# Performance work log

Measured on AMD Instinct MI355X. Metric: run time of the kernel, lower is better.

## Reference

```python
import jax, jax.numpy as jnp
import numpy as np

B, T, C = 2, 4096, 2048
N = 64
H = C // N
D_W, D_A, D_MV, D_G = 96, 96, 64, 256
LN_EPS = 0.00064


def setup_inputs() -> dict:
    key = jax.random.key(0)
    ks = jax.random.split(key, 32)
    rn = lambda k, shape, s=1.0: jax.random.normal(k, shape, jnp.float32) * s
    inp = {}
    inp["x"] = rn(ks[0], (B, T, C))
    inp["v_first"] = rn(ks[1], (B, T, C))
    # token-shift mixing coefficients (in (0,1) like 1 - ddd**p)
    for i, name in enumerate(["x_r", "x_w", "x_k", "x_v", "x_a", "x_g"]):
        inp[name] = jax.random.uniform(ks[2 + i], (1, 1, C), jnp.float32)
    # decay LoRA: w0 in roughly [-6, -0.5]
    inp["w0"] = jax.random.uniform(ks[8], (1, 1, C), jnp.float32, -6.0, -0.5)
    inp["w1"] = rn(ks[9], (C, D_W), 0.05)
    inp["w2"] = rn(ks[10], (D_W, C), 0.05)
    # in-context-learning-rate (a) LoRA
    inp["a0"] = rn(ks[11], (1, 1, C), 0.3) - 0.19
    inp["a1"] = rn(ks[12], (C, D_A), 0.05)
    inp["a2"] = rn(ks[13], (D_A, C), 0.05)
    # value-mix LoRA (layer_id > 0)
    inp["v0"] = rn(ks[14], (1, 1, C), 0.2) + 0.73
    inp["v1"] = rn(ks[15], (C, D_MV), 0.05)
    inp["v2"] = rn(ks[16], (D_MV, C), 0.05)
    # gate LoRA
    inp["g1"] = rn(ks[17], (C, D_G), 0.05)
    inp["g2"] = rn(ks[18], (D_G, C), 0.05)
    inp["k_k"] = rn(ks[19], (1, 1, C), 0.05) + 0.71
    inp["k_a"] = rn(ks[20], (1, 1, C), 0.02) + 1.02
    inp["r_k"] = rn(ks[21], (H, N), 0.02) - 0.04
    sc = 0.5 / C ** 0.5
    inp["W_r"] = jax.random.uniform(ks[22], (C, C), jnp.float32, -sc, sc)
    inp["W_k"] = jax.random.uniform(ks[23], (C, C), jnp.float32, -0.1 * sc, 0.1 * sc)
    inp["W_v"] = jax.random.uniform(ks[24], (C, C), jnp.float32, -sc, sc)
    inp["W_o"] = rn(ks[25], (C, C), 0.02)
    inp["ln_w"] = jnp.ones((C,), jnp.float32)
    inp["ln_b"] = jnp.zeros((C,), jnp.float32)
    return inp


def _wkv7(r, wdec, k, v, a, b):
    # r,wdec,k,v,a,b: [B,T,C]; per-head delta-rule scan, state S: [B,H,Nv,Nk]
    def heads(t):
        return t.reshape(B, T, H, N).transpose(1, 0, 2, 3)  # [T,B,H,N]

    def step(S, ins):
        r_t, w_t, k_t, v_t, a_t, b_t = ins  # each [B,H,N]
        sa = jnp.einsum('bhvk,bhk->bhv', S, a_t)
        S = (S * w_t[:, :, None, :]
             + sa[..., None] * b_t[:, :, None, :]
             + v_t[..., None] * k_t[:, :, None, :])
        y_t = jnp.einsum('bhvk,bhk->bhv', S, r_t)
        return S, y_t

    S0 = jnp.zeros((B, H, N, N), r.dtype)
    _, ys = jax.lax.scan(step, S0, (heads(r), heads(wdec), heads(k), heads(v), heads(a), heads(b)))
    return ys.transpose(1, 0, 2, 3).reshape(B, T, C)


def reference(x, v_first, x_r, x_w, x_k, x_v, x_a, x_g,
              w0, w1, w2, a0, a1, a2, v0, v1, v2, g1, g2,
              k_k, k_a, r_k, W_r, W_k, W_v, W_o, ln_w, ln_b):
    # token shift: prepend zero row, drop last
    xx = jnp.concatenate([jnp.zeros_like(x[:, :1]), x[:, :-1]], axis=1) - x
    xr = x + xx * x_r
    xw = x + xx * x_w
    xk = x + xx * x_k
    xv = x + xx * x_v
    xa = x + xx * x_a
    xg = x + xx * x_g
    r = xr @ W_r.T
    k = xk @ W_k.T
    v = xv @ W_v.T
    w = -jax.nn.softplus(-(w0 + jnp.tanh(xw @ w1) @ w2)) - 0.5
    # layer_id > 0: mix with first-layer value
    v = v + (v_first - v) * jax.nn.sigmoid(v0 + xv @ v1 @ v2)
    a = jax.nn.sigmoid(a0 + xa @ a1 @ a2)
    g = jax.nn.sigmoid(xg @ g1) @ g2
    kk = k * k_k
    kkh = kk.reshape(B, T, H, N)
    kkh = kkh / jnp.maximum(jnp.linalg.norm(kkh, axis=-1, keepdims=True), 1e-12)
    kk = kkh.reshape(B, T, C)
    k = k * (1.0 + (a - 1.0) * k_a)
    wdec = jnp.exp(-jnp.exp(w))  # RWKV7 decay parameterization
    y = _wkv7(r, wdec, k, v, -kk, kk * a)
    # GroupNorm(H groups) over channels per token
    yh = y.reshape(B, T, H, N)
    mu = yh.mean(-1, keepdims=True)
    var = yh.var(-1, keepdims=True)
    y = ((yh - mu) / jnp.sqrt(var + LN_EPS)).reshape(B, T, C) * ln_w + ln_b
    # bonus term
    rh, kh, vh = (t.reshape(B, T, H, N) for t in (r, k, v))
    bonus = ((rh * kh * r_k).sum(-1, keepdims=True) * vh).reshape(B, T, C)
    y = y + bonus
    return (y * g) @ W_o.T
```

## Files before the change

kernel.cpp:

```cpp
#include <hip/hip_runtime.h>
#include <hip/hip_bf16.h>
#include <stdint.h>
#include <math.h>

#define DEV __device__ __forceinline__

typedef __hip_bfloat16 bf16;
typedef __attribute__((ext_vector_type(8))) __bf16 bf16x8;
typedef __attribute__((ext_vector_type(4))) float f32x4;
typedef __attribute__((ext_vector_type(2))) float f32x2;

static constexpr int B_ = 2;
static constexpr int T_ = 4096;
static constexpr int C_ = 2048;
static constexpr int H_ = 32;

DEV void gld_lds16(const void* g, void* l) {
  __builtin_amdgcn_global_load_lds((const __attribute__((address_space(1))) void*)g,
                                   (__attribute__((address_space(3))) void*)l, 16, 0, 0);
}
DEV float bfbits2f(unsigned short u) {
  unsigned int x = ((unsigned int)u) << 16;
  return __builtin_bit_cast(float, x);
}
DEV unsigned short f2bfbits(float f) { bf16 h = __float2bfloat16(f); return __builtin_bit_cast(unsigned short, h); }
DEV void store_bf16x4(bf16* p, f32x4 v) {
  ushort4 u;
  u.x = f2bfbits(v.x); u.y = f2bfbits(v.y); u.z = f2bfbits(v.z); u.w = f2bfbits(v.w);
  *reinterpret_cast<ushort4*>(p) = u;
}
DEV float wsum64(float v) {
#pragma unroll
  for (int m = 32; m > 0; m >>= 1) v += __shfl_xor(v, m, 64);
  return v;
}
template<int CTRL>
DEV float dpp_add(float v) {
  int x = __builtin_bit_cast(int, v);
  int y = __builtin_amdgcn_update_dpp(0, x, CTRL, 0xf, 0xf, false);
  return v + __builtin_bit_cast(float, y);
}
DEV float red16(float v) {
  v = dpp_add<0xB1>(v);
  v = dpp_add<0x4E>(v);
  v = dpp_add<0x124>(v);
  v = dpp_add<0x128>(v);
  return v;
}
DEV f32x4 cvt4(uint2 u) {
  f32x4 o;
  o.x = __builtin_bit_cast(float, u.x << 16);
  o.y = __builtin_bit_cast(float, u.x & 0xFFFF0000u);
  o.z = __builtin_bit_cast(float, u.y << 16);
  o.w = __builtin_bit_cast(float, u.y & 0xFFFF0000u);
  return o;
}

template<int MODE>
__global__ __launch_bounds__(256)
void gemm_bt(const bf16* __restrict__ A, const bf16* __restrict__ Bm,
             void* __restrict__ Cout, const float* __restrict__ ep,
             int N, int K, int T4)
{
  __shared__ bf16 lA[128 * 64];
  __shared__ bf16 lB[128 * 64];
  const int tid  = threadIdx.x;
  const int wave = tid >> 6;
  const int lane = tid & 63;
  const long brow = (long)blockIdx.x * 128;
  const long bcol = (long)blockIdx.y * 128;
  const int wr = wave >> 1, wc = wave & 1;

  f32x4 acc[4][4];
#pragma unroll
  for (int m = 0; m < 4; ++m)
#pragma unroll
    for (int n = 0; n < 4; ++n)
      acc[m][n] = f32x4{0.f, 0.f, 0.f, 0.f};

  const bf16* pa = A  + (size_t)(brow + wave * 32 + (lane >> 3)) * K + (lane & 7) * 8;
  const bf16* pb = Bm + (size_t)(bcol + wave * 32 + (lane >> 3)) * K + (lane & 7) * 8;

  for (int k0 = 0; k0 < K; k0 += 64) {
#pragma unroll
    for (int i = 0; i < 4; ++i) gld_lds16(pa + (size_t)i * 8 * K, &lA[(wave * 4 + i) * 512]);
#pragma unroll
    for (int i = 0; i < 4; ++i) gld_lds16(pb + (size_t)i * 8 * K, &lB[(wave * 4 + i) * 512]);
    pa += 64; pb += 64;
    __syncthreads();
#pragma unroll
    for (int kk = 0; kk < 2; ++kk) {
      bf16x8 af[4], bfv[4];
#pragma unroll
      for (int m = 0; m < 4; ++m)
        af[m] = *(const bf16x8*)&lA[(wr * 64 + m * 16 + (lane & 15)) * 64 + kk * 32 + (lane >> 4) * 8];
#pragma unroll
      for (int n = 0; n < 4; ++n)
        bfv[n] = *(const bf16x8*)&lB[(wc * 64 + n * 16 + (lane & 15)) * 64 + kk * 32 + (lane >> 4) * 8];
#pragma unroll
      for (int m = 0; m < 4; ++m)
#pragma unroll
        for (int n = 0; n < 4; ++n)
          acc[m][n] = __builtin_amdgcn_mfma_f32_16x16x32_bf16(af[m], bfv[n], acc[m][n], 0, 0, 0);
    }
    __syncthreads();
  }

  const int cr = (lane >> 4) * 4;
  const int cc = lane & 15;
#pragma unroll
  for (int m = 0; m < 4; ++m) {
#pragma unroll
    for (int n = 0; n < 4; ++n) {
#pragma unroll
      for (int j = 0; j < 4; ++j) {
        long gm = brow + wr * 64 + m * 16 + cr + j;
        long gn = bcol + wc * 64 + n * 16 + cc;
        float val = acc[m][n][j];
        if constexpr (MODE == 0) {
          ((float*)Cout)[gm * N + gn] = val;
        } else if constexpr (MODE == 2) {
          ((bf16*)Cout)[gm * N + gn] = __float2bfloat16(val);
        } else if constexpr (MODE == 3) {
          ((bf16*)Cout)[gm * N + gn] = __float2bfloat16(tanhf(val));
        } else if constexpr (MODE == 4) {
          ((bf16*)Cout)[gm * N + gn] = __float2bfloat16(1.f / (1.f + expf(-val)));
        } else if constexpr (MODE == 7) {
          long b = gm / T4, t = gm % T4;
          ((bf16*)Cout)[((b * (N >> 6) + (gn >> 6)) * T4 + t) * 64 + (gn & 63)] = __float2bfloat16(val);
        } else if constexpr (MODE == 8) {
          float u = ep[gn] + val;
          float w = -log1pf(expf(-u)) - 0.5f;
          float wd = expf(-expf(w));
          long b = gm / T4, t = gm % T4;
          ((float*)Cout)[((b * (N >> 6) + (gn >> 6)) * T4 + t) * 64 + (gn & 63)] = wd;
        } else if constexpr (MODE == 9) {
          float sg = 1.f / (1.f + expf(-(ep[gn] + val)));
          long b = gm / T4, t = gm % T4;
          ((bf16*)Cout)[((b * (N >> 6) + (gn >> 6)) * T4 + t) * 64 + (gn & 63)] = __float2bfloat16(sg);
        }
      }
    }
  }
}

__global__ __launch_bounds__(256)
void mix1(const float* __restrict__ x, const float* __restrict__ coef,
          bf16* __restrict__ out)
{
  size_t e = ((size_t)blockIdx.x * 256 + threadIdx.x) * 4;
  int c = (int)(e & (C_ - 1));
  size_t m = e >> 11;
  f32x4 xc = *(const f32x4*)(x + e);
  f32x4 xp;
  if ((m & (T_ - 1)) == 0) xp = f32x4{0.f, 0.f, 0.f, 0.f};
  else                     xp = *(const f32x4*)(x + e - C_);
  f32x4 cf = *(const f32x4*)(coef + c);
  store_bf16x4(out + e, xc + (xp - xc) * cf);
}

__global__ __launch_bounds__(256)
void cvt1(const float* __restrict__ s, bf16* __restrict__ d)
{
  size_t e = ((size_t)blockIdx.x * 256 + threadIdx.x) * 4;
  store_bf16x4(d + e, *(const f32x4*)(s + e));
}

struct TPJob { const float* s; bf16* d; int R, Cs, NP, RP; };
struct TP8 { TPJob j[8]; };
__global__ __launch_bounds__(256)
void tpad(TP8 jobs)
{
  TPJob J = jobs.j[blockIdx.y];
  int i = blockIdx.x * 256 + threadIdx.x;
  int tot = J.NP * J.RP;
  if (i >= tot) return;
  int n = i / J.RP, r = i - n * J.RP;
  float v = (n < J.Cs && r < J.R) ? J.s[(size_t)r * J.Cs + n] : 0.f;
  J.d[i] = __float2bfloat16(v);
}

__global__ __launch_bounds__(256)
void prescan2(const bf16* __restrict__ r16, bf16* __restrict__ k16,
              bf16* __restrict__ v16, bf16* __restrict__ ab,
              bf16* __restrict__ vn16,
              const float* __restrict__ vfirst, const float* __restrict__ kkc,
              const float* __restrict__ kac, const float* __restrict__ rk,
              float* __restrict__ sbonus)
{
  const int wid = threadIdx.x >> 6;
  const int lane = threadIdx.x & 63;
  const long id = (long)blockIdx.x * 4 + wid;
  const long bh = id >> 12;
  const long t = id & (T_ - 1);
  const long b = bh >> 5, h = bh & (H_ - 1);
  const long mrow = b * T_ + t;
  const int c = (int)(h * 64 + lane);
  const size_t tp = (size_t)id * 64 + lane;
  float k  = __bfloat162float(k16[tp]);
  float v  = __bfloat162float(v16[tp]);
  float r  = __bfloat162float(r16[tp]);
  float a  = __bfloat162float(ab[tp]);
  float vs = __bfloat162float(vn16[tp]);
  float vf = vfirst[mrow * C_ + c];
  float kkv = k * kkc[c];
  float ssum = wsum64(kkv * kkv);
  float kkn = kkv / fmaxf(sqrtf(ssum), 1e-12f);
  float kn = k * (1.f + (a - 1.f) * kac[c]);
  float vn = v + (vf - v) * vs;
  k16[tp] = __float2bfloat16(kn);
  v16[tp] = __float2bfloat16(vn);
  ab[tp]  = __float2bfloat16(kkn * a);
  vn16[tp] = __float2bfloat16(kkn);
  float bs = wsum64(r * kn * rk[c]);
  if (lane == 0) sbonus[id] = bs;
}

struct SS {
  uint2 r0, r1, k0, k1, n0, n1, b0, b1;
  f32x4 w0, w1;
  unsigned short v0, v1;
};
DEV SS ldss(const uint2* pr, const uint2* pk, const uint2* pn, const uint2* pb,
            const f32x4* pw, const unsigned short* pv, int ss, int kq, int row)
{
  SS s;
  int i0 = ss * 32 + kq, i1 = i0 + 16;
  s.r0 = pr[i0]; s.r1 = pr[i1];
  s.k0 = pk[i0]; s.k1 = pk[i1];
  s.n0 = pn[i0]; s.n1 = pn[i1];
  s.b0 = pb[i0]; s.b1 = pb[i1];
  s.w0 = pw[i0]; s.w1 = pw[i1];
  int j0 = ss * 128 + row, j1 = j0 + 64;
  s.v0 = pv[j0]; s.v1 = pv[j1];
  return s;
}
DEV float dostep(f32x4& S, uint2 ru, uint2 ku, uint2 nu, uint2 bu,
                 f32x4 W, unsigned short vus)
{
  f32x4 R = cvt4(ru), K = cvt4(ku), N = cvt4(nu), Bv = cvt4(bu);
  float vt = bfbits2f(vus);
  f32x2 acc = S.xy * N.xy;
  acc = __builtin_elementwise_fma(S.zw, N.zw, acc);
  float sa = red16(acc.x + acc.y);
  float nsa = -sa;
  f32x2 ns2 = f32x2{nsa, nsa}, vt2 = f32x2{vt, vt};
  S.xy = __builtin_elementwise_fma(vt2, K.xy,
           __builtin_elementwise_fma(ns2, Bv.xy, S.xy * W.xy));
  S.zw = __builtin_elementwise_fma(vt2, K.zw,
           __builtin_elementwise_fma(ns2, Bv.zw, S.zw * W.zw));
  f32x2 yq = S.xy * R.xy;
  yq = __builtin_elementwise_fma(S.zw, R.zw, yq);
  return red16(yq.x + yq.y);
}
DEV void consume(f32x4& S, const SS& s, bf16* py, int t, int kq)
{
  float y0 = dostep(S, s.r0, s.k0, s.n0, s.b0, s.w0, s.v0);
  if (kq == 0) py[(size_t)t * 64] = __float2bfloat16(y0);
  float y1 = dostep(S, s.r1, s.k1, s.n1, s.b1, s.w1, s.v1);
  if (kq == 0) py[(size_t)(t + 1) * 64] = __float2bfloat16(y1);
}
__global__ __launch_bounds__(256, 1)
void wkv_scan5(const bf16* __restrict__ r16, const float* __restrict__ w32,
               const bf16* __restrict__ k16, const bf16* __restrict__ v16,
               const bf16* __restrict__ n16, const bf16* __restrict__ b16,
               bf16* __restrict__ y16)
{
  const int bh = blockIdx.x & 63;
  const int quarter = blockIdx.x >> 6;
  const int wv = threadIdx.x >> 6;
  const int lane = threadIdx.x & 63;
  const int vl = lane >> 4;
  const int kq = lane & 15;
  const int row = quarter * 16 + wv * 4 + vl;
  const size_t eb = (size_t)bh * (T_ * 64);
  const uint2* pr = (const uint2*)(r16 + eb);
  const uint2* pk = (const uint2*)(k16 + eb);
  const uint2* pn = (const uint2*)(n16 + eb);
  const uint2* pb = (const uint2*)(b16 + eb);
  const f32x4* pw = (const f32x4*)(w32 + eb);
  const unsigned short* pv = (const unsigned short*)(v16 + eb);
  bf16* py = y16 + eb + row;

  f32x4 S = f32x4{0.f, 0.f, 0.f, 0.f};
  const int NS = T_ / 2;

  SS s0 = ldss(pr, pk, pn, pb, pw, pv, 0, kq, row);
  SS s1 = ldss(pr, pk, pn, pb, pw, pv, 1, kq, row);
  SS s2 = ldss(pr, pk, pn, pb, pw, pv, 2, kq, row);
  SS s3 = ldss(pr, pk, pn, pb, pw, pv, 3, kq, row);

  for (int ss = 0; ss < NS; ss += 4) {
    int n0 = ss + 4 < NS ? ss + 4 : NS - 1;
    int n1 = ss + 5 < NS ? ss + 5 : NS - 1;
    int n2 = ss + 6 < NS ? ss + 6 : NS - 1;
    int n3 = ss + 7 < NS ? ss + 7 : NS - 1;
    SS p0 = ldss(pr, pk, pn, pb, pw, pv, n0, kq, row);
    consume(S, s0, py, 2 * ss, kq);
    SS p1 = ldss(pr, pk, pn, pb, pw, pv, n1, kq, row);
    consume(S, s1, py, 2 * ss + 2, kq);
    SS p2 = ldss(pr, pk, pn, pb, pw, pv, n2, kq, row);
    consume(S, s2, py, 2 * ss + 4, kq);
    SS p3 = ldss(pr, pk, pn, pb, pw, pv, n3, kq, row);
    consume(S, s3, py, 2 * ss + 6, kq);
    s0 = p0; s1 = p1; s2 = p2; s3 = p3;
  }
}

__global__ __launch_bounds__(256)
void postk2(const bf16* __restrict__ y16, const bf16* __restrict__ v16,
            const float* __restrict__ sbonus, const bf16* __restrict__ g16,
            const float* __restrict__ lnw, const float* __restrict__ lnb,
            bf16* __restrict__ opre)
{
  const int wid = threadIdx.x >> 6;
  const int lane = threadIdx.x & 63;
  const long id = (long)blockIdx.x * 4 + wid;
  const long bh = id >> 12;
  const long t = id & (T_ - 1);
  const long b = bh >> 5, h = bh & (H_ - 1);
  const long mrow = b * T_ + t;
  const int c = (int)(h * 64 + lane);
  const size_t tp = (size_t)id * 64 + lane;
  float y = __bfloat162float(y16[tp]);
  float mu = wsum64(y) * (1.f / 64.f);
  float d = y - mu;
  float var = wsum64(d * d) * (1.f / 64.f);
  float yn = d * rsqrtf(var + 0.00064f) * lnw[c] + lnb[c];
  float outv = (yn + sbonus[id] * __bfloat162float(v16[tp]))
               * __bfloat162float(g16[mrow * C_ + c]);
  opre[mrow * C_ + c] = __float2bfloat16(outv);
}

extern "C" void kernel_launch(void* const* d_in, const int* in_sizes, int n_in,
                              void* d_out, int out_size, void* d_ws, size_t ws_size,
                              hipStream_t stream)
{
  const float* x    = (const float*)d_in[0];
  const float* vfst = (const float*)d_in[1];
  const float* x_r  = (const float*)d_in[2];
  const float* x_w  = (const float*)d_in[3];
  const float* x_k  = (const float*)d_in[4];
  const float* x_v  = (const float*)d_in[5];
  const float* x_a  = (const float*)d_in[6];
  const float* x_g  = (const float*)d_in[7];
  const float* w0   = (const float*)d_in[8];
  const float* w1   = (const float*)d_in[9];
  const float* w2   = (const float*)d_in[10];
  const float* a0   = (const float*)d_in[11];
  const float* a1   = (const float*)d_in[12];
  const float* a2   = (const float*)d_in[13];
  const float* v0   = (const float*)d_in[14];
  const float* v1   = (const float*)d_in[15];
  const float* v2   = (const float*)d_in[16];
  const float* g1   = (const float*)d_in[17];
  const float* g2   = (const float*)d_in[18];
  const float* k_k  = (const float*)d_in[19];
  const float* k_a  = (const float*)d_in[20];
  const float* r_k  = (const float*)d_in[21];
  const float* W_r  = (const float*)d_in[22];
  const float* W_k  = (const float*)d_in[23];
  const float* W_v  = (const float*)d_in[24];
  const float* W_o  = (const float*)d_in[25];
  const float* lnw  = (const float*)d_in[26];
  const float* lnb  = (const float*)d_in[27];

  const size_t MB = 1048576ULL;
  const size_t HK = 524288ULL;
  if (ws_size < 248 * MB) return;

  char* ws = (char*)d_ws;
  bf16* r16  = (bf16*)(ws + 0 * MB);
  bf16* k16  = (bf16*)(ws + 32 * MB);
  bf16* v16  = (bf16*)(ws + 64 * MB);
  float* w32 = (float*)(ws + 96 * MB);
  bf16* opre = (bf16*)(ws + 96 * MB);
  bf16* asig = (bf16*)(ws + 160 * MB);
  bf16* vsig = (bf16*)(ws + 192 * MB);
  bf16* w1t = (bf16*)(ws + 224 * MB);
  bf16* a1t = (bf16*)(ws + 224 * MB + HK);
  bf16* v1t = (bf16*)(ws + 225 * MB);
  bf16* g1t = (bf16*)(ws + 225 * MB + HK);
  bf16* w2t = (bf16*)(ws + 226 * MB + HK);
  bf16* a2t = (bf16*)(ws + 227 * MB);
  bf16* v2t = (bf16*)(ws + 227 * MB + HK);
  bf16* g2t = (bf16*)(ws + 228 * MB);
  bf16* h_w = (bf16*)(ws + 229 * MB);
  bf16* h_a = (bf16*)(ws + 231 * MB);
  bf16* h_v = (bf16*)(ws + 233 * MB);
  bf16* h_g = (bf16*)(ws + 235 * MB);
  float* sb = (float*)(ws + 239 * MB);
  bf16* WB  = (bf16*)(ws + 240 * MB);
  bf16* g16 = (bf16*)d_out;
  bf16* MIX = (bf16*)((char*)d_out + 32 * MB);
  bf16* y16 = (bf16*)((char*)d_out + 32 * MB);

  TP8 jobs;
  jobs.j[0] = TPJob{ w1, w1t, 2048,   96,  128, 2048 };
  jobs.j[1] = TPJob{ a1, a1t, 2048,   96,  128, 2048 };
  jobs.j[2] = TPJob{ v1, v1t, 2048,   64,  128, 2048 };
  jobs.j[3] = TPJob{ g1, g1t, 2048,  256,  256, 2048 };
  jobs.j[4] = TPJob{ w2, w2t,   96, 2048, 2048,  128 };
  jobs.j[5] = TPJob{ a2, a2t,   96, 2048, 2048,  128 };
  jobs.j[6] = TPJob{ v2, v2t,   64, 2048, 2048,  128 };
  jobs.j[7] = TPJob{ g2, g2t,  256, 2048, 2048,  256 };
  tpad<<<dim3(2048, 8), 256, 0, stream>>>(jobs);

  mix1<<<dim3(16384), 256, 0, stream>>>(x, x_w, MIX);
  gemm_bt<3><<<dim3(64, 1), 256, 0, stream>>>(MIX, w1t, h_w, nullptr, 128, 2048, 0);
  mix1<<<dim3(16384), 256, 0, stream>>>(x, x_a, MIX);
  gemm_bt<2><<<dim3(64, 1), 256, 0, stream>>>(MIX, a1t, h_a, nullptr, 128, 2048, 0);
  mix1<<<dim3(16384), 256, 0, stream>>>(x, x_v, MIX);
  gemm_bt<2><<<dim3(64, 1), 256, 0, stream>>>(MIX, v1t, h_v, nullptr, 128, 2048, 0);
  mix1<<<dim3(16384), 256, 0, stream>>>(x, x_g, MIX);
  gemm_bt<4><<<dim3(64, 2), 256, 0, stream>>>(MIX, g1t, h_g, nullptr, 256, 2048, 0);

  gemm_bt<8><<<dim3(64, 16), 256, 0, stream>>>(h_w, w2t, w32, w0, 2048, 128, T_);
  gemm_bt<9><<<dim3(64, 16), 256, 0, stream>>>(h_a, a2t, asig, a0, 2048, 128, T_);
  gemm_bt<9><<<dim3(64, 16), 256, 0, stream>>>(h_v, v2t, vsig, v0, 2048, 128, T_);
  gemm_bt<2><<<dim3(64, 16), 256, 0, stream>>>(h_g, g2t, g16, nullptr, 2048, 256, 0);

  cvt1<<<dim3(4096), 256, 0, stream>>>(W_r, WB);
  mix1<<<dim3(16384), 256, 0, stream>>>(x, x_r, MIX);
  gemm_bt<7><<<dim3(64, 16), 256, 0, stream>>>(MIX, WB, r16, nullptr, 2048, 2048, T_);
  cvt1<<<dim3(4096), 256, 0, stream>>>(W_k, WB);
  mix1<<<dim3(16384), 256, 0, stream>>>(x, x_k, MIX);
  gemm_bt<7><<<dim3(64, 16), 256, 0, stream>>>(MIX, WB, k16, nullptr, 2048, 2048, T_);
  cvt1<<<dim3(4096), 256, 0, stream>>>(W_v, WB);
  mix1<<<dim3(16384), 256, 0, stream>>>(x, x_v, MIX);
  gemm_bt<7><<<dim3(64, 16), 256, 0, stream>>>(MIX, WB, v16, nullptr, 2048, 2048, T_);

  prescan2<<<dim3(65536), 256, 0, stream>>>(r16, k16, v16, asig, vsig,
                                            vfst, k_k, k_a, r_k, sb);
  wkv_scan5<<<dim3(256), 256, 0, stream>>>(r16, w32, k16, v16, vsig, asig, y16);
  postk2<<<dim3(65536), 256, 0, stream>>>(y16, v16, sb, g16, lnw, lnb, opre);

  cvt1<<<dim3(4096), 256, 0, stream>>>(W_o, WB);
  gemm_bt<0><<<dim3(64, 16), 256, 0, stream>>>(opre, WB, (float*)d_out, nullptr, 2048, 2048, 0);
}
```

Measured before the change: 1.952 ms.

## Interleave r/k and kk/b scan inputs into paired bf16 streams

```diff
diff --git a/kernel.cpp b/kernel.cpp
--- a/kernel.cpp
+++ b/kernel.cpp
@@ -18,16 +18,16 @@
 DEV void gld_lds16(const void* g, void* l) {
   __builtin_amdgcn_global_load_lds((const __attribute__((address_space(1))) void*)g,
                                    (__attribute__((address_space(3))) void*)l, 16, 0, 0);
-}
-DEV float bfbits2f(unsigned short u) {
-  unsigned int x = ((unsigned int)u) << 16;
-  return __builtin_bit_cast(float, x);
 }
 DEV unsigned short f2bfbits(float f) { bf16 h = __float2bfloat16(f); return __builtin_bit_cast(unsigned short, h); }
 DEV void store_bf16x4(bf16* p, f32x4 v) {
   ushort4 u;
   u.x = f2bfbits(v.x); u.y = f2bfbits(v.y); u.z = f2bfbits(v.z); u.w = f2bfbits(v.w);
   *reinterpret_cast<ushort4*>(p) = u;
+}
+DEV float bfbits2f(unsigned short u) {
+  unsigned int x = ((unsigned int)u) << 16;
+  return __builtin_bit_cast(float, x);
 }
 DEV float wsum64(float v) {
 #pragma unroll
@@ -47,14 +47,8 @@
   v = dpp_add<0x128>(v);
   return v;
 }
-DEV f32x4 cvt4(uint2 u) {
-  f32x4 o;
-  o.x = __builtin_bit_cast(float, u.x << 16);
-  o.y = __builtin_bit_cast(float, u.x & 0xFFFF0000u);
-  o.z = __builtin_bit_cast(float, u.y << 16);
-  o.w = __builtin_bit_cast(float, u.y & 0xFFFF0000u);
-  return o;
-}
+DEV float lo16f(unsigned int u) { return __builtin_bit_cast(float, u << 16); }
+DEV float hi16f(unsigned int u) { return __builtin_bit_cast(float, u & 0xFFFF0000u); }
 
 template<int MODE>
 __global__ __launch_bounds__(256)
@@ -125,19 +119,26 @@
           ((bf16*)Cout)[gm * N + gn] = __float2bfloat16(tanhf(val));
         } else if constexpr (MODE == 4) {
           ((bf16*)Cout)[gm * N + gn] = __float2bfloat16(1.f / (1.f + expf(-val)));
-        } else if constexpr (MODE == 7) {
+        } else {
           long b = gm / T4, t = gm % T4;
-          ((bf16*)Cout)[((b * (N >> 6) + (gn >> 6)) * T4 + t) * 64 + (gn & 63)] = __float2bfloat16(val);
-        } else if constexpr (MODE == 8) {
-          float u = ep[gn] + val;
-          float w = -log1pf(expf(-u)) - 0.5f;
-          float wd = expf(-expf(w));
-          long b = gm / T4, t = gm % T4;
-          ((float*)Cout)[((b * (N >> 6) + (gn >> 6)) * T4 + t) * 64 + (gn & 63)] = wd;
-        } else if constexpr (MODE == 9) {
-          float sg = 1.f / (1.f + expf(-(ep[gn] + val)));
-          long b = gm / T4, t = gm % T4;
-          ((bf16*)Cout)[((b * (N >> 6) + (gn >> 6)) * T4 + t) * 64 + (gn & 63)] = __float2bfloat16(sg);
+          long tidx = ((b * (N >> 6) + (gn >> 6)) * T4 + t) * 64 + (gn & 63);
+          if constexpr (MODE == 7) {
+            ((bf16*)Cout)[tidx] = __float2bfloat16(val);
+          } else if constexpr (MODE == 8) {
+            float u = ep[gn] + val;
+            float w = -log1pf(expf(-u)) - 0.5f;
+            ((float*)Cout)[tidx] = expf(-expf(w));
+          } else if constexpr (MODE == 9) {
+            float sg = 1.f / (1.f + expf(-(ep[gn] + val)));
+            ((bf16*)Cout)[tidx * 2] = __float2bfloat16(sg);
+          } else if constexpr (MODE == 10) {
+            float sg = 1.f / (1.f + expf(-(ep[gn] + val)));
+            ((bf16*)Cout)[tidx * 2 + 1] = __float2bfloat16(sg);
+          } else if constexpr (MODE == 11) {
+            ((bf16*)Cout)[tidx * 2] = __float2bfloat16(val);
+          } else if constexpr (MODE == 12) {
+            ((bf16*)Cout)[tidx * 2 + 1] = __float2bfloat16(val);
+          }
         }
       }
     }
@@ -181,11 +182,11 @@
 }
 
 __global__ __launch_bounds__(256)
-void prescan2(const bf16* __restrict__ r16, bf16* __restrict__ k16,
-              bf16* __restrict__ v16, bf16* __restrict__ ab,
-              bf16* __restrict__ vn16,
+void prescan3(bf16* __restrict__ rk,
+              bf16* __restrict__ v16,
+              bf16* __restrict__ av,
               const float* __restrict__ vfirst, const float* __restrict__ kkc,
-              const float* __restrict__ kac, const float* __restrict__ rk,
+              const float* __restrict__ kac, const float* __restrict__ rkc,
               float* __restrict__ sbonus)
 {
   const int wid = threadIdx.x >> 6;
@@ -197,73 +198,77 @@
   const long mrow = b * T_ + t;
   const int c = (int)(h * 64 + lane);
   const size_t tp = (size_t)id * 64 + lane;
-  float k  = __bfloat162float(k16[tp]);
+  const size_t tp2 = tp * 2;
+  float r  = __bfloat162float(rk[tp2]);
+  float k  = __bfloat162float(rk[tp2 + 1]);
+  float a  = __bfloat162float(av[tp2]);
+  float vs = __bfloat162float(av[tp2 + 1]);
   float v  = __bfloat162float(v16[tp]);
-  float r  = __bfloat162float(r16[tp]);
-  float a  = __bfloat162float(ab[tp]);
-  float vs = __bfloat162float(vn16[tp]);
   float vf = vfirst[mrow * C_ + c];
   float kkv = k * kkc[c];
   float ssum = wsum64(kkv * kkv);
   float kkn = kkv / fmaxf(sqrtf(ssum), 1e-12f);
   float kn = k * (1.f + (a - 1.f) * kac[c]);
   float vn = v + (vf - v) * vs;
-  k16[tp] = __float2bfloat16(kn);
+  rk[tp2 + 1] = __float2bfloat16(kn);
   v16[tp] = __float2bfloat16(vn);
-  ab[tp]  = __float2bfloat16(kkn * a);
-  vn16[tp] = __float2bfloat16(kkn);
-  float bs = wsum64(r * kn * rk[c]);
+  av[tp2]     = __float2bfloat16(kkn);
+  av[tp2 + 1] = __float2bfloat16(-(kkn * a));
+  float bs = wsum64(r * kn * rkc[c]);
   if (lane == 0) sbonus[id] = bs;
 }
 
 struct SS {
-  uint2 r0, r1, k0, k1, n0, n1, b0, b1;
+  uint4 rk0, rk1, nb0, nb1;
   f32x4 w0, w1;
   unsigned short v0, v1;
 };
-DEV SS ldss(const uint2* pr, const uint2* pk, const uint2* pn, const uint2* pb,
-            const f32x4* pw, const unsigned short* pv, int ss, int kq, int row)
+DEV SS ldss(const uint4* prk, const uint4* pnb, const f32x4* pw,
+            const unsigned short* pv, int ss, int kq, int row)
 {
   SS s;
   int i0 = ss * 32 + kq, i1 = i0 + 16;
-  s.r0 = pr[i0]; s.r1 = pr[i1];
-  s.k0 = pk[i0]; s.k1 = pk[i1];
-  s.n0 = pn[i0]; s.n1 = pn[i1];
-  s.b0 = pb[i0]; s.b1 = pb[i1];
+  s.rk0 = prk[i0]; s.rk1 = prk[i1];
+  s.nb0 = pnb[i0]; s.nb1 = pnb[i1];
   s.w0 = pw[i0]; s.w1 = pw[i1];
-  int j0 = ss * 128 + row, j1 = j0 + 64;
-  s.v0 = pv[j0]; s.v1 = pv[j1];
+  int j0 = ss * 128 + row;
+  s.v0 = pv[j0]; s.v1 = pv[j0 + 64];
   return s;
 }
-DEV float dostep(f32x4& S, uint2 ru, uint2 ku, uint2 nu, uint2 bu,
-                 f32x4 W, unsigned short vus)
-{
-  f32x4 R = cvt4(ru), K = cvt4(ku), N = cvt4(nu), Bv = cvt4(bu);
+DEV float dostep(f32x4& S, uint4 rk, uint4 nb, f32x4 W, unsigned short vus)
+{
+  f32x4 R, K, N, Bn;
+  R.x = lo16f(rk.x); K.x = hi16f(rk.x);
+  R.y = lo16f(rk.y); K.y = hi16f(rk.y);
+  R.z = lo16f(rk.z); K.z = hi16f(rk.z);
+  R.w = lo16f(rk.w); K.w = hi16f(rk.w);
+  N.x = lo16f(nb.x); Bn.x = hi16f(nb.x);
+  N.y = lo16f(nb.y); Bn.y = hi16f(nb.y);
+  N.z = lo16f(nb.z); Bn.z = hi16f(nb.z);
+  N.w = lo16f(nb.w); Bn.w = hi16f(nb.w);
   float vt = bfbits2f(vus);
   f32x2 acc = S.xy * N.xy;
   acc = __builtin_elementwise_fma(S.zw, N.zw, acc);
   float sa = red16(acc.x + acc.y);
-  float nsa = -sa;
-  f32x2 ns2 = f32x2{nsa, nsa}, vt2 = f32x2{vt, vt};
+  f32x2 sa2 = f32x2{sa, sa}, vt2 = f32x2{vt, vt};
   S.xy = __builtin_elementwise_fma(vt2, K.xy,
-           __builtin_elementwise_fma(ns2, Bv.xy, S.xy * W.xy));
+           __builtin_elementwise_fma(sa2, Bn.xy, S.xy * W.xy));
   S.zw = __builtin_elementwise_fma(vt2, K.zw,
-           __builtin_elementwise_fma(ns2, Bv.zw, S.zw * W.zw));
+           __builtin_elementwise_fma(sa2, Bn.zw, S.zw * W.zw));
   f32x2 yq = S.xy * R.xy;
   yq = __builtin_elementwise_fma(S.zw, R.zw, yq);
   return red16(yq.x + yq.y);
 }
 DEV void consume(f32x4& S, const SS& s, bf16* py, int t, int kq)
 {
-  float y0 = dostep(S, s.r0, s.k0, s.n0, s.b0, s.w0, s.v0);
+  float y0 = dostep(S, s.rk0, s.nb0, s.w0, s.v0);
   if (kq == 0) py[(size_t)t * 64] = __float2bfloat16(y0);
-  float y1 = dostep(S, s.r1, s.k1, s.n1, s.b1, s.w1, s.v1);
+  float y1 = dostep(S, s.rk1, s.nb1, s.w1, s.v1);
   if (kq == 0) py[(size_t)(t + 1) * 64] = __float2bfloat16(y1);
 }
 __global__ __launch_bounds__(256, 1)
-void wkv_scan5(const bf16* __restrict__ r16, const float* __restrict__ w32,
-               const bf16* __restrict__ k16, const bf16* __restrict__ v16,
-               const bf16* __restrict__ n16, const bf16* __restrict__ b16,
+void wkv_scan9(const bf16* __restrict__ rk16, const float* __restrict__ w32,
+               const bf16* __restrict__ nb16, const bf16* __restrict__ v16,
                bf16* __restrict__ y16)
 {
   const int bh = blockIdx.x & 63;
@@ -274,34 +279,32 @@
   const int kq = lane & 15;
   const int row = quarter * 16 + wv * 4 + vl;
   const size_t eb = (size_t)bh * (T_ * 64);
-  const uint2* pr = (const uint2*)(r16 + eb);
-  const uint2* pk = (const uint2*)(k16 + eb);
-  const uint2* pn = (const uint2*)(n16 + eb);
-  const uint2* pb = (const uint2*)(b16 + eb);
-  const f32x4* pw = (const f32x4*)(w32 + eb);
+  const uint4* prk = (const uint4*)(rk16 + eb * 2);
+  const uint4* pnb = (const uint4*)(nb16 + eb * 2);
+  const f32x4* pw  = (const f32x4*)(w32 + eb);
   const unsigned short* pv = (const unsigned short*)(v16 + eb);
   bf16* py = y16 + eb + row;
 
   f32x4 S = f32x4{0.f, 0.f, 0.f, 0.f};
   const int NS = T_ / 2;
 
-  SS s0 = ldss(pr, pk, pn, pb, pw, pv, 0, kq, row);
-  SS s1 = ldss(pr, pk, pn, pb, pw, pv, 1, kq, row);
-  SS s2 = ldss(pr, pk, pn, pb, pw, pv, 2, kq, row);
-  SS s3 = ldss(pr, pk, pn, pb, pw, pv, 3, kq, row);
+  SS s0 = ldss(prk, pnb, pw, pv, 0, kq, row);
+  SS s1 = ldss(prk, pnb, pw, pv, 1, kq, row);
+  SS s2 = ldss(prk, pnb, pw, pv, 2, kq, row);
+  SS s3 = ldss(prk, pnb, pw, pv, 3, kq, row);
 
   for (int ss = 0; ss < NS; ss += 4) {
     int n0 = ss + 4 < NS ? ss + 4 : NS - 1;
     int n1 = ss + 5 < NS ? ss + 5 : NS - 1;
     int n2 = ss + 6 < NS ? ss + 6 : NS - 1;
     int n3 = ss + 7 < NS ? ss + 7 : NS - 1;
-    SS p0 = ldss(pr, pk, pn, pb, pw, pv, n0, kq, row);
+    SS p0 = ldss(prk, pnb, pw, pv, n0, kq, row);
     consume(S, s0, py, 2 * ss, kq);
-    SS p1 = ldss(pr, pk, pn, pb, pw, pv, n1, kq, row);
+    SS p1 = ldss(prk, pnb, pw, pv, n1, kq, row);
     consume(S, s1, py, 2 * ss + 2, kq);
-    SS p2 = ldss(pr, pk, pn, pb, pw, pv, n2, kq, row);
+    SS p2 = ldss(prk, pnb, pw, pv, n2, kq, row);
     consume(S, s2, py, 2 * ss + 4, kq);
-    SS p3 = ldss(pr, pk, pn, pb, pw, pv, n3, kq, row);
+    SS p3 = ldss(prk, pnb, pw, pv, n3, kq, row);
     consume(S, s3, py, 2 * ss + 6, kq);
     s0 = p0; s1 = p1; s2 = p2; s3 = p3;
   }
@@ -370,13 +373,11 @@
   if (ws_size < 248 * MB) return;
 
   char* ws = (char*)d_ws;
-  bf16* r16  = (bf16*)(ws + 0 * MB);
-  bf16* k16  = (bf16*)(ws + 32 * MB);
+  bf16* rk16 = (bf16*)(ws + 0 * MB);
   bf16* v16  = (bf16*)(ws + 64 * MB);
   float* w32 = (float*)(ws + 96 * MB);
   bf16* opre = (bf16*)(ws + 96 * MB);
-  bf16* asig = (bf16*)(ws + 160 * MB);
-  bf16* vsig = (bf16*)(ws + 192 * MB);
+  bf16* av16 = (bf16*)(ws + 160 * MB);
   bf16* w1t = (bf16*)(ws + 224 * MB);
   bf16* a1t = (bf16*)(ws + 224 * MB + HK);
   bf16* v1t = (bf16*)(ws + 225 * MB);
@@ -415,24 +416,23 @@
   mix1<<<dim3(16384), 256, 0, stream>>>(x, x_g, MIX);
   gemm_bt<4><<<dim3(64, 2), 256, 0, stream>>>(MIX, g1t, h_g, nullptr, 256, 2048, 0);
 
-  gemm_bt<8><<<dim3(64, 16), 256, 0, stream>>>(h_w, w2t, w32, w0, 2048, 128, T_);
-  gemm_bt<9><<<dim3(64, 16), 256, 0, stream>>>(h_a, a2t, asig, a0, 2048, 128, T_);
-  gemm_bt<9><<<dim3(64, 16), 256, 0, stream>>>(h_v, v2t, vsig, v0, 2048, 128, T_);
-  gemm_bt<2><<<dim3(64, 16), 256, 0, stream>>>(h_g, g2t, g16, nullptr, 2048, 256, 0);
+  gemm_bt<8> <<<dim3(64, 16), 256, 0, stream>>>(h_w, w2t, w32,  w0, 2048, 128, T_);
+  gemm_bt<9> <<<dim3(64, 16), 256, 0, stream>>>(h_a, a2t, av16, a0, 2048, 128, T_);
+  gemm_bt<10><<<dim3(64, 16), 256, 0, stream>>>(h_v, v2t, av16, v0, 2048, 128, T_);
+  gemm_bt<2> <<<dim3(64, 16), 256, 0, stream>>>(h_g, g2t, g16, nullptr, 2048, 256, 0);
 
   cvt1<<<dim3(4096), 256, 0, stream>>>(W_r, WB);
   mix1<<<dim3(16384), 256, 0, stream>>>(x, x_r, MIX);
-  gemm_bt<7><<<dim3(64, 16), 256, 0, stream>>>(MIX, WB, r16, nullptr, 2048, 2048, T_);
+  gemm_bt<11><<<dim3(64, 16), 256, 0, stream>>>(MIX, WB, rk16, nullptr, 2048, 2048, T_);
   cvt1<<<dim3(4096), 256, 0, stream>>>(W_k, WB);
   mix1<<<dim3(16384), 256, 0, stream>>>(x, x_k, MIX);
-  gemm_bt<7><<<dim3(64, 16), 256, 0, stream>>>(MIX, WB, k16, nullptr, 2048, 2048, T_);
+  gemm_bt<12><<<dim3(64, 16), 256, 0, stream>>>(MIX, WB, rk16, nullptr, 2048, 2048, T_);
   cvt1<<<dim3(4096), 256, 0, stream>>>(W_v, WB);
   mix1<<<dim3(16384), 256, 0, stream>>>(x, x_v, MIX);
   gemm_bt<7><<<dim3(64, 16), 256, 0, stream>>>(MIX, WB, v16, nullptr, 2048, 2048, T_);
 
-  prescan2<<<dim3(65536), 256, 0, stream>>>(r16, k16, v16, asig, vsig,
-                                            vfst, k_k, k_a, r_k, sb);
-  wkv_scan5<<<dim3(256), 256, 0, stream>>>(r16, w32, k16, v16, vsig, asig, y16);
+  prescan3<<<dim3(65536), 256, 0, stream>>>(rk16, v16, av16, vfst, k_k, k_a, r_k, sb);
+  wkv_scan9<<<dim3(256), 256, 0, stream>>>(rk16, w32, av16, v16, y16);
   postk2<<<dim3(65536), 256, 0, stream>>>(y16, v16, sb, g16, lnw, lnb, opre);
 
   cvt1<<<dim3(4096), 256, 0, stream>>>(W_o, WB);
```

Result: faster. 1.896 ms (-2.9%).
